# Kernel tuning notes

Measured on AMD Instinct MI355X. Metric: run time of the kernel, lower is better.

Reference implementation:

```python
import jax, jax.numpy as jnp
import numpy as np


def setup_inputs() -> dict:
    key = jax.random.key(0)
    kx, kd = jax.random.split(key)
    B, C, T_phone = 32, 512, 1024
    x = jax.random.normal(kx, (B, C, T_phone), dtype=jnp.float32)
    durations = jax.random.randint(kd, (B, T_phone), 0, 8, dtype=jnp.int32)
    return {"x": x, "durations": durations}


def reference(x, durations):
    # x: [B, C, T_phone] float; durations: [B, T_phone] int
    B, C, T_phone = x.shape
    cum = jnp.cumsum(durations, axis=1)            # [B, T_phone] exclusive-end frame offsets
    total = cum[:, -1]                             # [B] total frames per utterance
    max_frames = int(jnp.max(total))               # T_frame (data-dependent, computed eagerly)
    t = jnp.arange(max_frames)                     # [T_frame]
    # frame t belongs to the first phone p with cum[b, p] > t (zero-duration phones skipped)
    p = jax.vmap(lambda c: jnp.searchsorted(c, t, side="right"))(cum)  # [B, T_frame]
    valid = t[None, :] < total[:, None]            # [B, T_frame] frames inside utterance
    p = jnp.clip(p, 0, T_phone - 1)
    idx = jnp.broadcast_to(p[:, None, :], (B, C, max_frames))
    out = jnp.take_along_axis(x, idx, axis=2)      # [B, C, T_frame] gather phone features
    out = jnp.where(valid[:, None, :], out, jnp.zeros((), dtype=x.dtype))
    mel_mask = ~valid                              # True where padding (matches torch ref)
    return out, mel_mask
```

## Files before the change

### kernel.cpp

```cpp
#include <hip/hip_runtime.h>

#define B 32
#define C 512
#define TP 1024
#define CHUNK 32

typedef float f4 __attribute__((ext_vector_type(4)));

__global__ void __launch_bounds__(256) cumsum_k(const int* __restrict__ dur,
                                                int* __restrict__ cum) {
    const int b = blockIdx.x, tid = threadIdx.x;
    const int lane = tid & 63, wid = tid >> 6;
    int4 v = ((const int4*)(dur + b * TP))[tid];
    const int s1 = v.x + v.y, s2 = s1 + v.z, s3 = s2 + v.w;
    int val = s3;
    #pragma unroll
    for (int off = 1; off < 64; off <<= 1) {
        int n = __shfl_up(val, off, 64);
        if (lane >= off) val += n;
    }
    __shared__ int wtot[4];
    if (lane == 63) wtot[wid] = val;
    __syncthreads();
    int base = 0;
    #pragma unroll
    for (int w = 0; w < 4; ++w)
        if (w < wid) base += wtot[w];
    const int excl = base + val - s3;
    int4 o;
    o.x = excl + v.x; o.y = excl + s1; o.z = excl + s2; o.w = excl + s3;
    ((int4*)(cum + b * TP))[tid] = o;
}

template <bool VEC>
__global__ void __launch_bounds__(256) gather_k(const float* __restrict__ x,
                                                const int* __restrict__ cum,
                                                float* __restrict__ out,
                                                float* __restrict__ mask,
                                                int MF) {
    __shared__ int scum[TP];
    const int b = blockIdx.y, z = blockIdx.z;
    ((int4*)scum)[threadIdx.x] = ((const int4*)(cum + b * TP))[threadIdx.x];
    __syncthreads();

    const int t0 = blockIdx.x * 1024 + threadIdx.x * 4;
    if (t0 >= MF) return;
    const int total = scum[TP - 1];

    int lo = 0, hi = TP;
    while (lo < hi) {
        int mid = (lo + hi) >> 1;
        if (scum[mid] <= t0) lo = mid + 1; else hi = mid;
    }
    int q[4]; bool val[4];
    int pc = lo;
    #pragma unroll
    for (int j = 0; j < 4; ++j) {
        const int tj = t0 + j;
        while (pc < TP && scum[pc] <= tj) ++pc;
        q[j] = pc < TP - 1 ? pc : TP - 1;
        val[j] = (tj < total) && (tj < MF);
    }

    const bool full = VEC && (t0 + 4 <= MF);

    if (z == 0) {
        float m[4];
        #pragma unroll
        for (int j = 0; j < 4; ++j) m[j] = (t0 + j < total) ? 0.0f : 1.0f;
        float* mrow = mask + (size_t)b * MF + t0;
        if (full) {
            f4 mv = {m[0], m[1], m[2], m[3]};
            __builtin_nontemporal_store(mv, (f4*)mrow);
        } else {
            #pragma unroll
            for (int j = 0; j < 4; ++j)
                if (t0 + j < MF) __builtin_nontemporal_store(m[j], mrow + j);
        }
    }

    const float* xb = x   + ((size_t)b * C + (size_t)z * CHUNK) * TP;
    float*       ob = out + ((size_t)b * C + (size_t)z * CHUNK) * MF;

    #pragma unroll 2
    for (int c = 0; c < CHUNK; ++c) {
        const float* xr = xb + (size_t)c * TP;
        float l0 = xr[q[0]], l1 = xr[q[1]], l2 = xr[q[2]], l3 = xr[q[3]];
        f4 v;
        v.x = val[0] ? l0 : 0.0f;
        v.y = val[1] ? l1 : 0.0f;
        v.z = val[2] ? l2 : 0.0f;
        v.w = val[3] ? l3 : 0.0f;
        float* orow = ob + (size_t)c * MF + t0;
        if (full) {
            __builtin_nontemporal_store(v, (f4*)orow);
        } else {
            const float vv[4] = {v.x, v.y, v.z, v.w};
            #pragma unroll
            for (int j = 0; j < 4; ++j)
                if (t0 + j < MF) __builtin_nontemporal_store(vv[j], orow + j);
        }
    }
}

extern "C" void kernel_launch(void* const* d_in, const int* in_sizes, int n_in,
                              void* d_out, int out_size, void* d_ws, size_t ws_size,
                              hipStream_t stream) {
    const float* x   = (const float*)d_in[0];
    const int*   dur = (const int*)d_in[1];
    float* out = (float*)d_out;

    const int MF = out_size / (B * (C + 1));
    float* mask = out + (size_t)B * C * MF;

    int* cum = (int*)d_ws;

    cumsum_k<<<B, 256, 0, stream>>>(dur, cum);

    dim3 ggrid((MF + 1023) / 1024, B, C / CHUNK);
    if ((MF & 3) == 0)
        gather_k<true><<<ggrid, 256, 0, stream>>>(x, cum, out, mask, MF);
    else
        gather_k<false><<<ggrid, 256, 0, stream>>>(x, cum, out, mask, MF);
}
```

Baseline: 323.7 us.

## Fuse cumsum into gather kernel and stage phone rows in LDS

Drops the separate cumsum launch: each gather block now computes the duration prefix sum itself in shared memory. Each block finds the phone range covering its frame tile, loads those rows of x into LDS with vectorized loads, and gathers from LDS instead of scattered global reads. Blocks lying entirely past the utterance end just write zeros, and CHUNK is halved to get more blocks. The cost is a redundant per-block prefix sum and extra LDS use, which may lower occupancy.

```diff
diff --git a/kernel.cpp b/kernel.cpp
--- a/kernel.cpp
+++ b/kernel.cpp
@@ -3,102 +3,176 @@
 #define B 32
 #define C 512
 #define TP 1024
-#define CHUNK 32
+#define CHUNK 16
+#define RMAX 432
+#define TTILE 1024
 
 typedef float f4 __attribute__((ext_vector_type(4)));
 
-__global__ void __launch_bounds__(256) cumsum_k(const int* __restrict__ dur,
-                                                int* __restrict__ cum) {
-    const int b = blockIdx.x, tid = threadIdx.x;
-    const int lane = tid & 63, wid = tid >> 6;
-    int4 v = ((const int4*)(dur + b * TP))[tid];
-    const int s1 = v.x + v.y, s2 = s1 + v.z, s3 = s2 + v.w;
-    int val = s3;
-    #pragma unroll
-    for (int off = 1; off < 64; off <<= 1) {
-        int n = __shfl_up(val, off, 64);
-        if (lane >= off) val += n;
+__device__ __forceinline__ int srch_right(const int* s, int t) {
+    int lo = 0, hi = TP;
+    while (lo < hi) {
+        int mid = (lo + hi) >> 1;
+        if (s[mid] <= t) lo = mid + 1; else hi = mid;
     }
-    __shared__ int wtot[4];
-    if (lane == 63) wtot[wid] = val;
-    __syncthreads();
-    int base = 0;
-    #pragma unroll
-    for (int w = 0; w < 4; ++w)
-        if (w < wid) base += wtot[w];
-    const int excl = base + val - s3;
-    int4 o;
-    o.x = excl + v.x; o.y = excl + s1; o.z = excl + s2; o.w = excl + s3;
-    ((int4*)(cum + b * TP))[tid] = o;
+    return lo;
 }
 
 template <bool VEC>
-__global__ void __launch_bounds__(256) gather_k(const float* __restrict__ x,
-                                                const int* __restrict__ cum,
-                                                float* __restrict__ out,
-                                                float* __restrict__ mask,
-                                                int MF) {
+__global__ void __launch_bounds__(256) lenreg_k(
+        const float* __restrict__ x, const int* __restrict__ dur,
+        float* __restrict__ out, float* __restrict__ mask, int MF) {
     __shared__ int scum[TP];
+    __shared__ float xs[CHUNK][RMAX];
+    __shared__ int wtot[4];
+
+    const int tid = threadIdx.x, lane = tid & 63, wid = tid >> 6;
     const int b = blockIdx.y, z = blockIdx.z;
-    ((int4*)scum)[threadIdx.x] = ((const int4*)(cum + b * TP))[threadIdx.x];
+
+    int4 d4 = ((const int4*)(dur + b * TP))[tid];
+    const int s1 = d4.x + d4.y, s2 = s1 + d4.z, s3 = s2 + d4.w;
+    int v = s3;
+    #pragma unroll
+    for (int off = 1; off < 64; off <<= 1) {
+        int n = __shfl_up(v, off, 64);
+        if (lane >= off) v += n;
+    }
+    if (lane == 63) wtot[wid] = v;
+    __syncthreads();
+    int bse = 0;
+    #pragma unroll
+    for (int w = 0; w < 4; ++w) if (w < wid) bse += wtot[w];
+    const int excl = bse + v - s3;
+    int4 o; o.x = excl + d4.x; o.y = excl + s1; o.z = excl + s2; o.w = excl + s3;
+    ((int4*)scum)[tid] = o;
     __syncthreads();
 
-    const int t0 = blockIdx.x * 1024 + threadIdx.x * 4;
-    if (t0 >= MF) return;
     const int total = scum[TP - 1];
+    const int tb0 = blockIdx.x * TTILE;
+    const bool blk_valid = total > tb0;
 
-    int lo = 0, hi = TP;
-    while (lo < hi) {
-        int mid = (lo + hi) >> 1;
-        if (scum[mid] <= t0) lo = mid + 1; else hi = mid;
-    }
-    int q[4]; bool val[4];
-    int pc = lo;
-    #pragma unroll
-    for (int j = 0; j < 4; ++j) {
-        const int tj = t0 + j;
-        while (pc < TP && scum[pc] <= tj) ++pc;
-        q[j] = pc < TP - 1 ? pc : TP - 1;
-        val[j] = (tj < total) && (tj < MF);
+    int p0a = 0, Ra = 0;
+    bool stage = false;
+    if (blk_valid) {
+        const int t_hi = min(min(tb0 + TTILE, total), MF) - 1;
+        const int p_lo = srch_right(scum, tb0);
+        const int p_hi = srch_right(scum, t_hi);
+        p0a = p_lo & ~3;
+        Ra = p_hi - p0a + 1;
+        stage = (Ra <= RMAX);
     }
 
-    const bool full = VEC && (t0 + 4 <= MF);
+    const float* xb = x + ((size_t)b * C + (size_t)z * CHUNK) * TP;
 
-    if (z == 0) {
-        float m[4];
+    if (stage) {
+        const int nf4 = (Ra + 3) >> 2;
         #pragma unroll
-        for (int j = 0; j < 4; ++j) m[j] = (t0 + j < total) ? 0.0f : 1.0f;
-        float* mrow = mask + (size_t)b * MF + t0;
-        if (full) {
-            f4 mv = {m[0], m[1], m[2], m[3]};
-            __builtin_nontemporal_store(mv, (f4*)mrow);
-        } else {
-            #pragma unroll
-            for (int j = 0; j < 4; ++j)
-                if (t0 + j < MF) __builtin_nontemporal_store(m[j], mrow + j);
+        for (int rr = 0; rr < CHUNK / 4; ++rr) {
+            const int r = rr * 4 + wid;
+            const float* xr = xb + (size_t)r * TP + p0a;
+            for (int i = lane; i < nf4; i += 64) {
+                f4 t4 = ((const f4*)xr)[i];
+                *((f4*)&xs[r][i * 4]) = t4;
+            }
         }
     }
 
-    const float* xb = x   + ((size_t)b * C + (size_t)z * CHUNK) * TP;
-    float*       ob = out + ((size_t)b * C + (size_t)z * CHUNK) * MF;
+    const int t0 = tb0 + tid * 4;
+    const bool active = t0 < MF;
+    const bool full = VEC && (t0 + 4 <= MF);
 
-    #pragma unroll 2
-    for (int c = 0; c < CHUNK; ++c) {
-        const float* xr = xb + (size_t)c * TP;
-        float l0 = xr[q[0]], l1 = xr[q[1]], l2 = xr[q[2]], l3 = xr[q[3]];
-        f4 v;
-        v.x = val[0] ? l0 : 0.0f;
-        v.y = val[1] ? l1 : 0.0f;
-        v.z = val[2] ? l2 : 0.0f;
-        v.w = val[3] ? l3 : 0.0f;
-        float* orow = ob + (size_t)c * MF + t0;
-        if (full) {
-            __builtin_nontemporal_store(v, (f4*)orow);
+    int q[4]; bool vld[4]; int ix[4];
+    if (active) {
+        if (blk_valid) {
+            int pc = srch_right(scum, t0);
+            #pragma unroll
+            for (int j = 0; j < 4; ++j) {
+                const int tj = t0 + j;
+                while (pc < TP && scum[pc] <= tj) ++pc;
+                q[j] = pc < TP - 1 ? pc : TP - 1;
+                vld[j] = (tj < total) && (tj < MF);
+                ix[j] = vld[j] ? q[j] - p0a : 0;
+            }
         } else {
-            const float vv[4] = {v.x, v.y, v.z, v.w};
             #pragma unroll
-            for (int j = 0; j < 4; ++j)
-                if (t0 + j < MF) __builtin_nontemporal_store(vv[j], orow + j);
+            for (int j = 0; j < 4; ++j) { q[j] = TP - 1; vld[j] = false; ix[j] = 0; }
+        }
+        if (z == 0) {
+            float m[4];
+            #pragma unroll
+            for (int j = 0; j < 4; ++j) m[j] = (t0 + j < total) ? 0.0f : 1.0f;
+            float* mrow = mask + (size_t)b * MF + t0;
+            if (full) {
+                f4 mv = {m[0], m[1], m[2], m[3]};
+                __builtin_nontemporal_store(mv, (f4*)mrow);
+            } else {
+                #pragma unroll
+                for (int j = 0; j < 4; ++j)
+                    if (t0 + j < MF) __builtin_nontemporal_store(m[j], mrow + j);
+            }
+        }
+    }
+
+    if (stage) __syncthreads();
+    if (!active) return;
+
+    float* ob = out + ((size_t)b * C + (size_t)z * CHUNK) * MF;
+
+    if (!blk_valid) {
+        const f4 zz = {0.0f, 0.0f, 0.0f, 0.0f};
+        #pragma unroll 4
+        for (int c = 0; c < CHUNK; ++c) {
+            float* orow = ob + (size_t)c * MF + t0;
+            if (full) {
+                __builtin_nontemporal_store(zz, (f4*)orow);
+            } else {
+                #pragma unroll
+                for (int j = 0; j < 4; ++j)
+                    if (t0 + j < MF) __builtin_nontemporal_store(0.0f, orow + j);
+            }
+        }
+        return;
+    }
+
+    if (stage) {
+        #pragma unroll 2
+        for (int c = 0; c < CHUNK; ++c) {
+            float l0 = xs[c][ix[0]], l1 = xs[c][ix[1]],
+                  l2 = xs[c][ix[2]], l3 = xs[c][ix[3]];
+            f4 v4;
+            v4.x = vld[0] ? l0 : 0.0f;
+            v4.y = vld[1] ? l1 : 0.0f;
+            v4.z = vld[2] ? l2 : 0.0f;
+            v4.w = vld[3] ? l3 : 0.0f;
+            float* orow = ob + (size_t)c * MF + t0;
+            if (full) {
+                __builtin_nontemporal_store(v4, (f4*)orow);
+            } else {
+                const float vv[4] = {v4.x, v4.y, v4.z, v4.w};
+                #pragma unroll
+                for (int j = 0; j < 4; ++j)
+                    if (t0 + j < MF) __builtin_nontemporal_store(vv[j], orow + j);
+            }
+        }
+    } else {
+        #pragma unroll 2
+        for (int c = 0; c < CHUNK; ++c) {
+            const float* xr = xb + (size_t)c * TP;
+            float l0 = xr[q[0]], l1 = xr[q[1]], l2 = xr[q[2]], l3 = xr[q[3]];
+            f4 v4;
+            v4.x = vld[0] ? l0 : 0.0f;
+            v4.y = vld[1] ? l1 : 0.0f;
+            v4.z = vld[2] ? l2 : 0.0f;
+            v4.w = vld[3] ? l3 : 0.0f;
+            float* orow = ob + (size_t)c * MF + t0;
+            if (full) {
+                __builtin_nontemporal_store(v4, (f4*)orow);
+            } else {
+                const float vv[4] = {v4.x, v4.y, v4.z, v4.w};
+                #pragma unroll
+                for (int j = 0; j < 4; ++j)
+                    if (t0 + j < MF) __builtin_nontemporal_store(vv[j], orow + j);
+            }
         }
     }
 }
@@ -113,13 +187,9 @@
     const int MF = out_size / (B * (C + 1));
     float* mask = out + (size_t)B * C * MF;
 
-    int* cum = (int*)d_ws;
-
-    cumsum_k<<<B, 256, 0, stream>>>(dur, cum);
-
-    dim3 ggrid((MF + 1023) / 1024, B, C / CHUNK);
+    dim3 g((MF + TTILE - 1) / TTILE, B, C / CHUNK);
     if ((MF & 3) == 0)
-        gather_k<true><<<ggrid, 256, 0, stream>>>(x, cum, out, mask, MF);
+        lenreg_k<true><<<g, 256, 0, stream>>>(x, dur, out, mask, MF);
     else
-        gather_k<false><<<ggrid, 256, 0, stream>>>(x, cum, out, mask, MF);
+        lenreg_k<false><<<g, 256, 0, stream>>>(x, dur, out, mask, MF);
 }
```

New measurement: 307.9 us. -4.9%, faster.
